# Kernel tuning notes

Hardware: AMD Instinct MI355X
Metric: run time of the kernel (lower is better)

Reference implementation:

```python
import jax, jax.numpy as jnp
import numpy as np

SCALE = 1.0 / np.sqrt(768.0).astype(np.float32)


def setup_inputs() -> dict:
    key = jax.random.key(0)
    k1, k2, k3, k4, k5 = jax.random.split(key, 5)
    B, LQ, LK, D = 32, 18, 4096, 768
    Q = jax.random.normal(k1, (B, LQ, D), dtype=jnp.float32)
    K = jax.random.normal(k2, (B, LK, D), dtype=jnp.float32)
    V = jax.random.normal(k3, (B, LK, D), dtype=jnp.float32)
    attn_mask = jax.random.randint(k4, (B, LQ, LK), 0, 2).astype(jnp.bool_)
    # fc: nn.Linear(18, 1, bias=False) -> weight [1, 18]
    W = jax.random.normal(k5, (1, 18), dtype=jnp.float32) * (1.0 / np.sqrt(18.0))
    return {"Q": Q, "K": K, "V": V, "attn_mask": attn_mask, "W": W}


def reference(Q, K, V, attn_mask, W):
    # scores: [B, 18, LK]
    scores = jnp.einsum("bqd,bkd->bqk", Q, K) * SCALE
    scores = jnp.where(attn_mask, jnp.float32(-1e9), scores)
    attn = jax.nn.softmax(scores, axis=-1)              # [B, 18, LK]
    # fc on attn^T: [B, LK, 18] @ W^T -> [B, LK, 1]
    attn_fc = jnp.einsum("bqk,oq->bko", attn, W)        # [B, LK, 1]
    # context: attn_fc^T @ V -> [B, 1, D]
    context = jnp.einsum("bko,bkd->bod", attn_fc, V)    # [B, 1, D]
    return context, attn_fc
```

## Files before the change

kernel.cpp:

```cpp
#include <hip/hip_runtime.h>
#include <hip/hip_bf16.h>

#define BB 32
#define LQ 18
#define LK 4096
#define DD 768
#define SCALE 0.03608439182435161f

#define WS_P       0
#define WS_PARTIAL 9437184
#define WS_WQD     9584640
#define WS_FLAG    9586944

#define DK 32
#define NT (DD / DK)

#define GLD16(gp, lp) __builtin_amdgcn_global_load_lds(                      \
    (const __attribute__((address_space(1))) void*)(gp),                     \
    (__attribute__((address_space(3))) void*)(lp), 16, 0, 0)

__global__ void detect_kernel(const unsigned char* __restrict__ m,
                              int* __restrict__ flag) {
    __shared__ int cnt;
    if (threadIdx.x == 0) cnt = 0;
    __syncthreads();
    int c = 0;
    for (int i = threadIdx.x; i < 16384; i += 256) {
        if ((i & 3) != 0 && m[i] != 0) c = 1;
    }
    if (c) atomicAdd(&cnt, 1);
    __syncthreads();
    if (threadIdx.x == 0) *flag = (cnt == 0) ? 1 : 0;
}

__global__ __launch_bounds__(256, 2) void qk_softmax_kernel(
    const float* __restrict__ Qg, const float* __restrict__ Kg,
    const void* __restrict__ maskg, const int* __restrict__ flag,
    float* __restrict__ P, float* __restrict__ partial) {
    const int chunk = blockIdx.x;
    const int b     = blockIdx.y;
    const int tid   = threadIdx.x;
    const int k     = chunk * 256 + tid;

    __shared__ float kt[2][256 * DK];

    const float* Kb = Kg + ((size_t)b * LK + (size_t)chunk * 256) * DD;
    const float* Qb = Qg + (size_t)b * LQ * DD;

    float acc[LQ];
#pragma unroll
    for (int q = 0; q < LQ; ++q) acc[q] = 0.0f;

    auto stage = [&](float* dst, int d0) {
#pragma unroll
        for (int i = 0; i < 8; ++i) {
            const int s   = i * 256 + tid;
            const int row = s >> 3;
            const int c   = s & 7;
            const float* src = Kb + (size_t)row * DD + d0 + ((c ^ (row & 7)) << 2);
            GLD16(src, dst + s * 4);
        }
    };

    stage(kt[0], 0);

    const int sw = tid & 7;

    for (int t = 0; t < NT; ++t) {
        float* buf = kt[t & 1];
        if (t + 1 < NT) {
            stage(kt[(t + 1) & 1], (t + 1) * DK);
            asm volatile("s_waitcnt vmcnt(8)" ::: "memory");
        } else {
            asm volatile("s_waitcnt vmcnt(0)" ::: "memory");
        }
        __builtin_amdgcn_s_barrier();
        asm volatile("" ::: "memory");

        float4 kv[8];
#pragma unroll
        for (int c = 0; c < 8; ++c)
            kv[c] = *(const float4*)(buf + tid * DK + ((c ^ sw) << 2));

        const int d0 = t * DK;
#pragma unroll
        for (int q = 0; q < LQ; ++q) {
            const float* Qr = Qb + q * DD + d0;
#pragma unroll
            for (int c = 0; c < 8; ++c) {
                const float4 qv = *(const float4*)(Qr + (c << 2));
                acc[q] += qv.x * kv[c].x;
                acc[q] += qv.y * kv[c].y;
                acc[q] += qv.z * kv[c].z;
                acc[q] += qv.w * kv[c].w;
            }
        }
        asm volatile("s_waitcnt lgkmcnt(0)" ::: "memory");
        __builtin_amdgcn_s_barrier();
        asm volatile("" ::: "memory");
    }

    const int isI32 = *flag;
    const unsigned char* m8  = (const unsigned char*)maskg;
    const int*           m32 = (const int*)maskg;

    float p[LQ];
#pragma unroll
    for (int q = 0; q < LQ; ++q) {
        const size_t idx = ((size_t)b * LQ + q) * LK + k;
        const int msk = isI32 ? m32[idx] : (int)m8[idx];
        const float pv = msk ? 0.0f : __expf(acc[q] * SCALE);
        p[q] = pv;
        P[idx] = pv;
    }

    const int lane = tid & 63;
    const int wv   = tid >> 6;
#pragma unroll
    for (int q = 0; q < LQ; ++q) {
        float s = p[q];
#pragma unroll
        for (int off = 32; off > 0; off >>= 1) s += __shfl_xor(s, off, 64);
        if (lane == 0)
            partial[((size_t)b * LQ + q) * 64 + (chunk * 4 + wv)] = s;
    }
}

__global__ void denom_kernel(const float* __restrict__ partial,
                             const float* __restrict__ Wg,
                             float* __restrict__ wqd) {
    const int b = blockIdx.x;
    const int q = threadIdx.x;
    if (q < LQ) {
        const float* pp = partial + ((size_t)b * LQ + q) * 64;
        float s = 0.0f;
#pragma unroll
        for (int w = 0; w < 64; ++w) s += pp[w];
        wqd[b * LQ + q] = Wg[q] / s;
    }
}

__global__ __launch_bounds__(256, 2) void fc_context_kernel(
    const float* __restrict__ P, const float* __restrict__ Vg,
    const float* __restrict__ wqd, float* __restrict__ ctx_out,
    float* __restrict__ af_out) {
    const int chunk = blockIdx.x;
    const int b     = blockIdx.y;
    const int tid   = threadIdx.x;
    const int k0    = chunk * 256;

    __shared__ float af_s[256];

    {
        const int k = k0 + tid;
        float af = 0.0f;
#pragma unroll
        for (int q = 0; q < LQ; ++q) {
            af += P[((size_t)b * LQ + q) * LK + k] * wqd[b * LQ + q];
        }
        af_s[tid] = af;
        af_out[(size_t)b * LK + k] = af;
    }
    __syncthreads();

    if (tid < 192) {
        const int d = tid << 2;
        const float* Vb = Vg + ((size_t)b * LK + k0) * DD + d;
        float cx = 0.0f, cy = 0.0f, cz = 0.0f, cw = 0.0f;
#pragma unroll 8
        for (int j = 0; j < 256; ++j) {
            const float  a = af_s[j];
            const float4 v = *(const float4*)(Vb + (size_t)j * DD);
            cx += a * v.x;
            cy += a * v.y;
            cz += a * v.z;
            cw += a * v.w;
        }
        float* cp = ctx_out + b * DD + d;
        atomicAdd(cp + 0, cx);
        atomicAdd(cp + 1, cy);
        atomicAdd(cp + 2, cz);
        atomicAdd(cp + 3, cw);
    }
}

extern "C" void kernel_launch(void* const* d_in, const int* in_sizes, int n_in,
                              void* d_out, int out_size, void* d_ws, size_t ws_size,
                              hipStream_t stream) {
    const float* Qg   = (const float*)d_in[0];
    const float* Kg   = (const float*)d_in[1];
    const float* Vg   = (const float*)d_in[2];
    const void*  mask = d_in[3];
    const float* Wg   = (const float*)d_in[4];

    float* ctx_out = (float*)d_out;
    float* af_out  = (float*)d_out + BB * DD;

    char*  ws      = (char*)d_ws;
    float* P       = (float*)(ws + WS_P);
    float* partial = (float*)(ws + WS_PARTIAL);
    float* wqd     = (float*)(ws + WS_WQD);
    int*   flag    = (int*)(ws + WS_FLAG);

    hipMemsetAsync(d_out, 0, BB * DD * sizeof(float), stream);

    detect_kernel<<<1, 256, 0, stream>>>((const unsigned char*)mask, flag);
    qk_softmax_kernel<<<dim3(16, BB), 256, 0, stream>>>(Qg, Kg, mask, flag, P, partial);
    denom_kernel<<<BB, 64, 0, stream>>>(partial, Wg, wqd);
    fc_context_kernel<<<dim3(16, BB), 256, 0, stream>>>(P, Vg, wqd, ctx_out, af_out);
}
```

Baseline: 900.8 us.

## Stage Q in LDS and split K rows across 8-lane groups in QK kernel

The QK/softmax kernel now loads the batch's whole Q matrix into shared memory once and has each group of 8 threads share 4 K rows. Each thread reads K directly from global memory in coalesced 16-byte chunks, with no LDS double-buffering of K. Partial dot products are combined with intra-group shuffles, and each block covers 128 keys instead of 256, so the grid doubles and the partial-sum buffer shrinks to 32 entries per row. This removes the repeated global/scalar reads of Q and the K staging barriers. In exchange it uses about 55KB of LDS per block, which limits occupancy, and adds shuffle reductions.

```diff
diff --git a/kernel.cpp b/kernel.cpp
--- a/kernel.cpp
+++ b/kernel.cpp
@@ -9,11 +9,8 @@
 
 #define WS_P       0
 #define WS_PARTIAL 9437184
-#define WS_WQD     9584640
-#define WS_FLAG    9586944
-
-#define DK 32
-#define NT (DD / DK)
+#define WS_WQD     9510912
+#define WS_FLAG    9513216
 
 #define GLD16(gp, lp) __builtin_amdgcn_global_load_lds(                      \
     (const __attribute__((address_space(1))) void*)(gp),                     \
@@ -37,92 +34,98 @@
     const float* __restrict__ Qg, const float* __restrict__ Kg,
     const void* __restrict__ maskg, const int* __restrict__ flag,
     float* __restrict__ P, float* __restrict__ partial) {
-    const int chunk = blockIdx.x;
-    const int b     = blockIdx.y;
-    const int tid   = threadIdx.x;
-    const int k     = chunk * 256 + tid;
-
-    __shared__ float kt[2][256 * DK];
-
-    const float* Kb = Kg + ((size_t)b * LK + (size_t)chunk * 256) * DD;
-    const float* Qb = Qg + (size_t)b * LQ * DD;
-
-    float acc[LQ];
-#pragma unroll
-    for (int q = 0; q < LQ; ++q) acc[q] = 0.0f;
-
-    auto stage = [&](float* dst, int d0) {
-#pragma unroll
-        for (int i = 0; i < 8; ++i) {
-            const int s   = i * 256 + tid;
-            const int row = s >> 3;
-            const int c   = s & 7;
-            const float* src = Kb + (size_t)row * DD + d0 + ((c ^ (row & 7)) << 2);
-            GLD16(src, dst + s * 4);
-        }
-    };
-
-    stage(kt[0], 0);
-
-    const int sw = tid & 7;
-
-    for (int t = 0; t < NT; ++t) {
-        float* buf = kt[t & 1];
-        if (t + 1 < NT) {
-            stage(kt[(t + 1) & 1], (t + 1) * DK);
-            asm volatile("s_waitcnt vmcnt(8)" ::: "memory");
-        } else {
-            asm volatile("s_waitcnt vmcnt(0)" ::: "memory");
-        }
-        __builtin_amdgcn_s_barrier();
-        asm volatile("" ::: "memory");
-
-        float4 kv[8];
-#pragma unroll
-        for (int c = 0; c < 8; ++c)
-            kv[c] = *(const float4*)(buf + tid * DK + ((c ^ sw) << 2));
-
-        const int d0 = t * DK;
+    const int bx  = blockIdx.x;
+    const int b   = blockIdx.y;
+    const int tid = threadIdx.x;
+    const int r   = tid >> 3;
+    const int c   = tid & 7;
+
+    __shared__ float qs[LQ * DD];
+    __shared__ float part[4][LQ];
+
+    {
+        const float* Qb = Qg + (size_t)b * LQ * DD;
+        for (int i = tid; i < (LQ * DD) / 4; i += 256)
+            GLD16(Qb + i * 4, qs + i * 4);
+    }
+    asm volatile("s_waitcnt vmcnt(0)" ::: "memory");
+    __syncthreads();
+
+    float acc[4][LQ];
+#pragma unroll
+    for (int j = 0; j < 4; ++j)
+#pragma unroll
+        for (int q = 0; q < LQ; ++q) acc[j][q] = 0.0f;
+
+    const float* K0 = Kg + ((size_t)b * LK + bx * 128 + r) * DD + (c << 2);
+
+    for (int t = 0; t < DD / 32; ++t) {
+        float4 kv[4];
+#pragma unroll
+        for (int j = 0; j < 4; ++j)
+            kv[j] = *(const float4*)(K0 + (size_t)j * 32 * DD + t * 32);
 #pragma unroll
         for (int q = 0; q < LQ; ++q) {
-            const float* Qr = Qb + q * DD + d0;
-#pragma unroll
-            for (int c = 0; c < 8; ++c) {
-                const float4 qv = *(const float4*)(Qr + (c << 2));
-                acc[q] += qv.x * kv[c].x;
-                acc[q] += qv.y * kv[c].y;
-                acc[q] += qv.z * kv[c].z;
-                acc[q] += qv.w * kv[c].w;
+            const float4 qv = *(const float4*)(qs + q * DD + t * 32 + (c << 2));
+#pragma unroll
+            for (int j = 0; j < 4; ++j) {
+                acc[j][q] += qv.x * kv[j].x;
+                acc[j][q] += qv.y * kv[j].y;
+                acc[j][q] += qv.z * kv[j].z;
+                acc[j][q] += qv.w * kv[j].w;
             }
         }
-        asm volatile("s_waitcnt lgkmcnt(0)" ::: "memory");
-        __builtin_amdgcn_s_barrier();
-        asm volatile("" ::: "memory");
-    }
+    }
+
+#pragma unroll
+    for (int j = 0; j < 4; ++j)
+#pragma unroll
+        for (int q = 0; q < LQ; ++q) {
+            float s = acc[j][q];
+            s += __shfl_xor(s, 1, 64);
+            s += __shfl_xor(s, 2, 64);
+            s += __shfl_xor(s, 4, 64);
+            acc[j][q] = s;
+        }
 
     const int isI32 = *flag;
     const unsigned char* m8  = (const unsigned char*)maskg;
     const int*           m32 = (const int*)maskg;
 
-    float p[LQ];
+    float dsum[3] = {0.0f, 0.0f, 0.0f};
 #pragma unroll
     for (int q = 0; q < LQ; ++q) {
-        const size_t idx = ((size_t)b * LQ + q) * LK + k;
-        const int msk = isI32 ? m32[idx] : (int)m8[idx];
-        const float pv = msk ? 0.0f : __expf(acc[q] * SCALE);
-        p[q] = pv;
-        P[idx] = pv;
-    }
-
-    const int lane = tid & 63;
-    const int wv   = tid >> 6;
-#pragma unroll
-    for (int q = 0; q < LQ; ++q) {
-        float s = p[q];
-#pragma unroll
-        for (int off = 32; off > 0; off >>= 1) s += __shfl_xor(s, off, 64);
-        if (lane == 0)
-            partial[((size_t)b * LQ + q) * 64 + (chunk * 4 + wv)] = s;
+        if ((q & 7) == c) {
+#pragma unroll
+            for (int j = 0; j < 4; ++j) {
+                const int    k   = bx * 128 + (j << 5) + r;
+                const size_t idx = ((size_t)b * LQ + q) * LK + k;
+                const int    msk = isI32 ? m32[idx] : (int)m8[idx];
+                const float  pv  = msk ? 0.0f : __expf(acc[j][q] * SCALE);
+                P[idx] = pv;
+                dsum[q >> 3] += pv;
+            }
+        }
+    }
+
+#pragma unroll
+    for (int i = 0; i < 3; ++i) {
+        float s = dsum[i];
+        s += __shfl_xor(s, 8, 64);
+        s += __shfl_xor(s, 16, 64);
+        s += __shfl_xor(s, 32, 64);
+        dsum[i] = s;
+    }
+    const int w = tid >> 6;
+    if ((tid & 63) < 8) {
+        part[w][c]     = dsum[0];
+        part[w][c + 8] = dsum[1];
+        if (c < 2) part[w][c + 16] = dsum[2];
+    }
+    __syncthreads();
+    if (tid < LQ) {
+        partial[((size_t)b * LQ + tid) * 32 + bx] =
+            part[0][tid] + part[1][tid] + part[2][tid] + part[3][tid];
     }
 }
 
@@ -132,10 +135,10 @@
     const int b = blockIdx.x;
     const int q = threadIdx.x;
     if (q < LQ) {
-        const float* pp = partial + ((size_t)b * LQ + q) * 64;
+        const float* pp = partial + ((size_t)b * LQ + q) * 32;
         float s = 0.0f;
 #pragma unroll
-        for (int w = 0; w < 64; ++w) s += pp[w];
+        for (int w = 0; w < 32; ++w) s += pp[w];
         wqd[b * LQ + q] = Wg[q] / s;
     }
 }
@@ -205,7 +208,7 @@
     hipMemsetAsync(d_out, 0, BB * DD * sizeof(float), stream);
 
     detect_kernel<<<1, 256, 0, stream>>>((const unsigned char*)mask, flag);
-    qk_softmax_kernel<<<dim3(16, BB), 256, 0, stream>>>(Qg, Kg, mask, flag, P, partial);
+    qk_softmax_kernel<<<dim3(32, BB), 256, 0, stream>>>(Qg, Kg, mask, flag, P, partial);
     denom_kernel<<<BB, 64, 0, stream>>>(partial, Wg, wqd);
     fc_context_kernel<<<dim3(16, BB), 256, 0, stream>>>(P, Vg, wqd, ctx_out, af_out);
 }
```

After: 854.8 us. 5.1% less time.
